# Performance work log

Measured on AMD Instinct MI355X. Metric: run time of the kernel, lower is better.

The kernel has to match this reference:

```python
import jax, jax.numpy as jnp
import numpy as np

N_P, N_W, F_IN = 512, 3584, 256
H1, O1 = 8, 32
H2, O2 = 8, 256
BATCH = 1024
NEG_SLOPE = 0.2


def _xavier(key, shape):
    fan_in, fan_out = shape[-2], shape[-1]
    lim = jnp.sqrt(6.0 / (fan_in + fan_out))
    return jax.random.uniform(key, shape, jnp.float32, -lim, lim)


def setup_inputs() -> dict:
    key = jax.random.key(0)
    ks = jax.random.split(key, 16)
    return {
        "input": jax.random.uniform(ks[0], (BATCH, N_W), jnp.float32),
        "pern_feature": jax.random.normal(ks[1], (N_P, F_IN), jnp.float32),
        "word_feature": jax.random.normal(ks[2], (N_W, F_IN), jnp.float32),
        "w1": _xavier(ks[3], (H1, F_IN, O1)),
        "a_src1": _xavier(ks[4], (H1, O1, 1)),
        "a_dst1": _xavier(ks[5], (H1, O1, 1)),
        "b1": jnp.zeros((O1,), jnp.float32),
        "w2": _xavier(ks[6], (H2, F_IN, O2)),
        "a_src2": _xavier(ks[7], (H2, F_IN, 1)),
        "a_dst2": _xavier(ks[8], (H2, F_IN, 1)),
        "b2": jnp.zeros((O2,), jnp.float32),
        "W_fc": _xavier(ks[9], (O2, 5)),
        "b_fc": jnp.zeros((5,), jnp.float32),
        "pern_adj": jax.random.randint(ks[10], (N_P, N_P), 0, 2, jnp.int32),
        "word_pern_adj": jax.random.randint(ks[11], (N_P + N_W, N_P + N_W), 0, 2, jnp.int32),
    }


def gat(h, adj, w, a_src, a_dst, bias):
    # h: [N, f_in], adj: [N, N] int, w: [H, f_in, f_out]
    h_prime = jnp.einsum('nf,hfo->hno', h, w)          # [H, N, O]
    t = jnp.tanh(h_prime)
    s_src = jnp.einsum('hno,hoi->hn', t, a_src)        # [H, N]
    s_dst = jnp.einsum('hno,hoi->hn', t, a_dst)        # [H, N]
    attn = s_src[:, :, None] + s_dst[:, None, :]       # [H, N, N]
    attn = jnp.where(attn >= 0, attn, NEG_SLOPE * attn)  # leaky_relu
    attn = jnp.where(adj[None, :, :] > 0, attn, -jnp.inf)
    attn = jax.nn.softmax(attn, axis=-1)
    out = jnp.einsum('hnm,hmo->hno', attn, h_prime)    # [H, N, O]
    return out + bias


def reference(input, pern_feature, word_feature, w1, a_src1, a_dst1, b1,
              w2, a_src2, a_dst2, b2, W_fc, b_fc, pern_adj, word_pern_adj):
    n_p = pern_feature.shape[0]
    # GAT 1 over personality graph
    h1 = gat(pern_feature, pern_adj, w1, a_src1, a_dst1, b1)       # [H1, n_p, O1]
    hiddn_pp = jnp.transpose(h1, (1, 0, 2)).reshape(n_p, -1)        # [n_p, H1*O1]
    hiddn_pp = jax.nn.elu(hiddn_pp)
    # dropout is identity in eval mode
    hiddn_wp = jnp.concatenate([word_feature, hiddn_pp], axis=0)    # [N, 256]
    h2 = gat(hiddn_wp, word_pern_adj, w2, a_src2, a_dst2, b2)       # [H2, N, O2]
    hiddn_wp2 = h2.mean(axis=0)                                     # [N, O2]
    hiddn_w = hiddn_wp2[:word_feature.shape[0], :]                  # [n_w, O2]
    x = (input @ hiddn_w) / input.sum(axis=1, keepdims=True)        # [B, O2]
    return x @ W_fc + b_fc                                          # [B, 5]
```

## Files before the change

### kernel.cpp

```cpp
#include <hip/hip_runtime.h>
#include <hip/hip_bf16.h>
#include <math.h>

#define NP 512
#define NW 3584
#define NT 4096
#define FIN 256
#define H1 8
#define O1 32
#define H2 8
#define O2 256
#define NEG 0.2f

typedef __attribute__((ext_vector_type(8))) short bf16x8;
typedef __attribute__((ext_vector_type(4))) float f32x4;
typedef __attribute__((ext_vector_type(2))) float v2f;
typedef unsigned long long u64;

__device__ __forceinline__ unsigned short f2bf(float f) {
    unsigned u = __float_as_uint(f);
    unsigned r = (u + 0x7FFF + ((u >> 16) & 1)) >> 16;
    return (unsigned short)r;
}

__device__ __forceinline__ float fast_tanh(float x) {
    float ex = __expf(2.0f * x);
    return 1.0f - 2.0f / (ex + 1.0f);
}

__global__ __launch_bounds__(256) void k_prep(
    const float* __restrict__ wf, const float* __restrict__ pf,
    const float* __restrict__ w1, const float* __restrict__ a_src1,
    const float* __restrict__ a_dst1, const float* __restrict__ w2,
    const float* __restrict__ b2, const float* __restrict__ W_fc,
    const int* __restrict__ wp_adj,
    unsigned short* __restrict__ abf, unsigned short* __restrict__ btbf,
    float* __restrict__ hp1, float* __restrict__ ss1, float* __restrict__ sd1,
    u64* __restrict__ maskT64, float* __restrict__ cvec)
{
    __shared__ float tile[64][65];
    __shared__ float feat[2][FIN];
    __shared__ float red[4][5];
    int blk = blockIdx.x;
    int t = threadIdx.x;
    if (blk < 896) {
        int idx4 = blk * 256 + t;
        float4 x = ((const float4*)wf)[idx4];
        ushort4 y;
        y.x = f2bf(x.x); y.y = f2bf(x.y); y.z = f2bf(x.z); y.w = f2bf(x.w);
        ((ushort4*)abf)[idx4] = y;
    } else if (blk < 1152) {
        int n0 = (blk - 896) * 2;
        feat[0][t] = pf[n0 * FIN + t];
        feat[1][t] = pf[(n0 + 1) * FIN + t];
        __syncthreads();
        int h = t >> 5, o = t & 31;
        float acc0 = 0.f, acc1 = 0.f;
        const float* wcol = w1 + h * FIN * O1 + o;
        #pragma unroll 4
        for (int f = 0; f < FIN; f++) {
            float w = wcol[f * O1];
            acc0 += feat[0][f] * w;
            acc1 += feat[1][f] * w;
        }
        hp1[n0 * 256 + t] = acc0;
        hp1[(n0 + 1) * 256 + t] = acc1;
        float as = a_src1[h * O1 + o];
        float ad = a_dst1[h * O1 + o];
        float accs[2] = {acc0, acc1};
        #pragma unroll
        for (int i = 0; i < 2; i++) {
            float th = tanhf(accs[i]);
            float vs = th * as, vd = th * ad;
            #pragma unroll
            for (int off = 1; off < 32; off <<= 1) {
                vs += __shfl_xor(vs, off);
                vd += __shfl_xor(vd, off);
            }
            if (o == 0) { ss1[h * NP + n0 + i] = vs; sd1[h * NP + n0 + i] = vd; }
        }
    } else if (blk < 1280) {
        int blk2 = blk - 1152;
        int h = blk2 >> 4;
        int f0 = ((blk2 >> 2) & 3) * 64;
        int o0 = (blk2 & 3) * 64;
        #pragma unroll
        for (int rr = 0; rr < 16; rr++) {
            int f = rr * 4 + (t >> 6);
            int o = t & 63;
            tile[f][o] = w2[((size_t)(h * FIN + f0 + f)) * O2 + o0 + o];
        }
        __syncthreads();
        #pragma unroll
        for (int rr = 0; rr < 16; rr++) {
            int o = rr * 4 + (t >> 6);
            int f = t & 63;
            btbf[((size_t)(h * O2 + o0 + o)) * FIN + f0 + f] = f2bf(tile[f][o]);
        }
    } else if (blk < 2176) {
        int w = t >> 6, l = t & 63;
        int r = (blk - 1280) * 4 + w;
        const int4* row = (const int4*)(wp_adj + (size_t)r * NT);
        for (int c4 = 0; c4 < 16; c4++) {
            int4 x = row[c4 * 64 + l];
            u64 nib = (u64)((x.x != 0 ? 1 : 0) | (x.y != 0 ? 2 : 0) |
                            (x.z != 0 ? 4 : 0) | (x.w != 0 ? 8 : 0));
            u64 v = nib << (4 * (l & 15));
            v |= __shfl_xor(v, 1);
            v |= __shfl_xor(v, 2);
            v |= __shfl_xor(v, 4);
            v |= __shfl_xor(v, 8);
            if ((l & 15) == 0) {
                int qw = c4 * 4 + (l >> 4);
                maskT64[(size_t)qw * NW + r] = v;
            }
        }
    } else {
        float v[5];
        #pragma unroll
        for (int j = 0; j < 5; j++) v[j] = b2[t] * W_fc[t * 5 + j];
        #pragma unroll
        for (int off = 1; off < 64; off <<= 1)
            #pragma unroll
            for (int j = 0; j < 5; j++) v[j] += __shfl_xor(v[j], off);
        int w = t >> 6, l = t & 63;
        if (l == 0) { for (int j = 0; j < 5; j++) red[w][j] = v[j]; }
        __syncthreads();
        if (t == 0)
            for (int j = 0; j < 5; j++) cvec[j] = red[0][j] + red[1][j] + red[2][j] + red[3][j];
    }
}

__global__ __launch_bounds__(256) void k_gat1_attn(
    const int* __restrict__ adj, const float* __restrict__ hp1,
    const float* __restrict__ ss1, const float* __restrict__ sd1,
    const float* __restrict__ b1, unsigned short* __restrict__ abf)
{
    __shared__ float p[2][H1][NP];
    __shared__ float den[2][H1];
    int t = threadIdx.x;
    int n0 = blockIdx.x * 2;
    for (int rr = 0; rr < 32; rr++) {
        int idx = rr * 256 + t;
        int i = idx >> 12, h = (idx >> 9) & 7, m = idx & 511;
        float a = adj[(n0 + i) * NP + m] > 0 ? 1.0f : 0.0f;
        float e = ss1[h * NP + n0 + i] + sd1[h * NP + m];
        e = fmaxf(e, NEG * e);
        p[i][h][m] = a * __expf(e);
    }
    __syncthreads();
    int w = t >> 6, l = t & 63;
    {
        int i = w & 1;
        #pragma unroll
        for (int hh = 0; hh < 4; hh++) {
            int h = (w >> 1) * 4 + hh;
            float s = 0;
            #pragma unroll
            for (int q = 0; q < 8; q++) s += p[i][h][l + 64 * q];
            #pragma unroll
            for (int off = 1; off < 64; off <<= 1) s += __shfl_xor(s, off);
            if (l == 0) den[i][h] = s;
        }
    }
    __syncthreads();
    int h = t >> 5, o = t & 31;
    float a0a = 0.f, a0b = 0.f, a1a = 0.f, a1b = 0.f;
    #pragma unroll 8
    for (int m = 0; m < NP; m += 2) {
        float v0 = hp1[m * 256 + t];
        float v1 = hp1[(m + 1) * 256 + t];
        a0a += p[0][h][m] * v0;
        a1a += p[1][h][m] * v0;
        a0b += p[0][h][m + 1] * v1;
        a1b += p[1][h][m + 1] * v1;
    }
    float acc[2] = {a0a + a0b, a1a + a1b};
    float bo = b1[o];
    #pragma unroll
    for (int i = 0; i < 2; i++) {
        float r = acc[i] / den[i][h] + bo;
        r = r > 0.f ? r : expm1f(r);
        abf[(NW + n0 + i) * FIN + t] = f2bf(r);
    }
}

__global__ __launch_bounds__(256) void k_gemm_hp2(
    const unsigned short* __restrict__ abf, const unsigned short* __restrict__ btbf,
    const float* __restrict__ a_src2, const float* __restrict__ a_dst2,
    const float* __restrict__ W_fc, float* __restrict__ gpart)
{
    __shared__ unsigned short As[128][264];
    int b = blockIdx.x;
    int nt = b & 1, h = (b >> 1) & 7, mt = b >> 4;
    int t = threadIdx.x;
    int w = t >> 6, l = t & 63;
    int m0 = mt * 128;
    {
        int row = t >> 5;
        int col8 = (t & 31) * 8;
        #pragma unroll
        for (int u = 0; u < 16; u++)
            *(bf16x8*)(&As[u * 8 + row][col8]) =
                *(const bf16x8*)(abf + (size_t)(m0 + u * 8 + row) * FIN + col8);
    }
    __syncthreads();
    int am0 = (w >> 1) * 64;
    int n0 = nt * 128 + (w & 1) * 64;
    int lr = l & 15, lq = l >> 4;
    const unsigned short* bbase = btbf + h * O2 * FIN;
    f32x4 acc[4][4];
    #pragma unroll
    for (int i = 0; i < 4; i++)
        #pragma unroll
        for (int j = 0; j < 4; j++) acc[i][j] = (f32x4){0.f, 0.f, 0.f, 0.f};
    #pragma unroll
    for (int k = 0; k < FIN; k += 32) {
        bf16x8 a[4], bf[4];
        int kc = k + lq * 8;
        #pragma unroll
        for (int j = 0; j < 4; j++)
            bf[j] = *(const bf16x8*)(bbase + (size_t)(n0 + j * 16 + lr) * FIN + kc);
        #pragma unroll
        for (int i = 0; i < 4; i++)
            a[i] = *(const bf16x8*)(&As[am0 + i * 16 + lr][kc]);
        #pragma unroll
        for (int i = 0; i < 4; i++)
            #pragma unroll
            for (int j = 0; j < 4; j++)
                acc[i][j] = __builtin_amdgcn_mfma_f32_16x16x32_bf16(a[i], bf[j], acc[i][j], 0, 0, 0);
    }
    int slice = nt * 2 + (w & 1);
    float as[4], ad[4], wfc[4][5];
    #pragma unroll
    for (int j = 0; j < 4; j++) {
        int col = n0 + j * 16 + lr;
        as[j] = a_src2[h * O2 + col];
        ad[j] = a_dst2[h * O2 + col];
        #pragma unroll
        for (int jj = 0; jj < 5; jj++) wfc[j][jj] = W_fc[col * 5 + jj];
    }
    float* base = gpart + ((size_t)h * 4 + slice) * NT * 8;
    #pragma unroll
    for (int i = 0; i < 4; i++) {
        #pragma unroll
        for (int r = 0; r < 4; r++) {
            float s[7] = {0,0,0,0,0,0,0};
            #pragma unroll
            for (int j = 0; j < 4; j++) {
                float x = acc[i][j][r];
                float th = fast_tanh(x);
                s[0] += th * as[j];
                s[1] += th * ad[j];
                #pragma unroll
                for (int jj = 0; jj < 5; jj++) s[2 + jj] += x * wfc[j][jj];
            }
            #pragma unroll
            for (int off = 1; off < 16; off <<= 1)
                #pragma unroll
                for (int q = 0; q < 7; q++) s[q] += __shfl_xor(s[q], off);
            if (lr == 0) {
                int m = m0 + am0 + i * 16 + lq * 4 + r;
                float* dst = base + (size_t)m * 8;
                #pragma unroll
                for (int q = 0; q < 7; q++) dst[q] = s[q];
            }
        }
    }
}

__global__ __launch_bounds__(256) void k_comb_hp2(
    const float* __restrict__ gpart,
    float* __restrict__ Etab, float* __restrict__ Eptab, float* __restrict__ T)
{
    int idx = blockIdx.x * 256 + threadIdx.x;
    float s[7] = {0,0,0,0,0,0,0};
    #pragma unroll
    for (int sl = 0; sl < 4; sl++) {
        const float* p = gpart + (((size_t)(idx >> 12) * 4 + sl) * NT + (idx & (NT - 1))) * 8;
        #pragma unroll
        for (int q = 0; q < 7; q++) s[q] += p[q];
    }
    Etab[idx]  = __expf(s[0]);
    Eptab[idx] = __expf(NEG * s[0]);
    float4 t0 = {__expf(s[1]), __expf(NEG * s[1]), 1.0f, s[2]};
    float4 t1 = {s[3], s[4], s[5], s[6]};
    *(float4*)(T + (size_t)idx * 8)     = t0;
    *(float4*)(T + (size_t)idx * 8 + 4) = t1;
}

__global__ __launch_bounds__(256) void k_gat2_attn(
    const u64* __restrict__ maskT64, const float* __restrict__ Etab,
    const float* __restrict__ Eptab, const float* __restrict__ T,
    float* __restrict__ part)
{
    int t = threadIdx.x;
    int w = t >> 6, l = t & 63;
    int b = blockIdx.x;
    int nb = b % 112;
    int h  = (b / 112) & 7;
    int c  = b / 896;
    int n0 = __builtin_amdgcn_readfirstlane(nb * 32 + w * 8);
    u64 epk[8];
    #pragma unroll
    for (int i = 0; i < 8; i++) {
        int r = h * NT + n0 + i;
        unsigned e  = __builtin_amdgcn_readfirstlane(__float_as_uint(Etab[r]));
        unsigned ep = __builtin_amdgcn_readfirstlane(__float_as_uint(Eptab[r]));
        epk[i] = ((u64)ep << 32) | e;
    }
    float den[8] = {0,0,0,0,0,0,0,0};
    float num[8][5] = {{0}};
    const float* Th = T + ((size_t)h * NT + c * 2048) * 8;
    for (int q = 0; q < 32; q++) {
        const float* tp = Th + (size_t)(q * 64 + l) * 8;
        f32x4 t0 = *(const f32x4*)tp;
        f32x4 t1 = *(const f32x4*)(tp + 4);
        v2f ffp = {t0.x, t0.y};
        size_t moff = (size_t)(c * 32 + q) * NW + n0;
        const u64* mq = maskT64 + moff;
        #pragma unroll
        for (int i = 0; i < 8; i++) {
            u64 wv = mq[i];
            unsigned wlo = __builtin_amdgcn_readfirstlane((unsigned)wv);
            unsigned whi = __builtin_amdgcn_readfirstlane((unsigned)(wv >> 32));
            u64 word = ((u64)whi << 32) | wlo;
            v2f pab;
            asm("v_pk_mul_f32 %0, %1, %2" : "=v"(pab) : "v"(ffp), "s"(epk[i]));
            float pp0 = fmaxf(pab.x, pab.y);
            float pp;
            asm("v_cndmask_b32 %0, 0, %1, %2" : "=v"(pp) : "v"(pp0), "s"(word));
            den[i] += pp;
            num[i][0] = fmaf(pp, t0.w, num[i][0]);
            num[i][1] = fmaf(pp, t1.x, num[i][1]);
            num[i][2] = fmaf(pp, t1.y, num[i][2]);
            num[i][3] = fmaf(pp, t1.z, num[i][3]);
            num[i][4] = fmaf(pp, t1.w, num[i][4]);
        }
    }
    #pragma unroll
    for (int i = 0; i < 8; i++) {
        float v[6];
        v[0] = den[i];
        #pragma unroll
        for (int j = 0; j < 5; j++) v[1 + j] = num[i][j];
        #pragma unroll
        for (int off = 1; off < 8; off <<= 1)
            #pragma unroll
            for (int k = 0; k < 6; k++) v[k] += __shfl_xor(v[k], off);
        if ((l & 7) == 0) {
            float* dst = part + ((((size_t)c * NW + n0 + i) * 8 + h) * 8 + (l >> 3)) * 8;
            #pragma unroll
            for (int k = 0; k < 6; k++) dst[k] = v[k];
        }
    }
}

__global__ __launch_bounds__(256) void k_gat2_comb(const float* __restrict__ part,
                                                   float* __restrict__ hf) {
    int idx = blockIdx.x * 256 + threadIdx.x;
    int n = idx >> 3, h = idx & 7;
    float den = 0, num[5] = {0,0,0,0,0};
    #pragma unroll
    for (int cc = 0; cc < 2; cc++) {
        #pragma unroll
        for (int s = 0; s < 8; s++) {
            const float* p = part + ((((size_t)cc * NW + n) * 8 + h) * 8 + s) * 8;
            float4 a = *(const float4*)p;
            float4 bq = *(const float4*)(p + 4);
            den += a.x;
            num[0] += a.y; num[1] += a.z; num[2] += a.w;
            num[3] += bq.x; num[4] += bq.y;
        }
    }
    float inv = 1.0f / (den * 8.0f);
    float v[5];
    #pragma unroll
    for (int j = 0; j < 5; j++) v[j] = num[j] * inv;
    #pragma unroll
    for (int off = 1; off < 8; off <<= 1)
        #pragma unroll
        for (int j = 0; j < 5; j++) v[j] += __shfl_xor(v[j], off);
    if (h == 0) {
        #pragma unroll
        for (int j = 0; j < 5; j++) hf[n * 5 + j] = v[j];
    }
}

__global__ __launch_bounds__(256) void k_final(
    const float* __restrict__ input, const float* __restrict__ hf,
    const float* __restrict__ cvec, const float* __restrict__ b_fc,
    float* __restrict__ out)
{
    int b = blockIdx.x, t = threadIdx.x;
    const float4* row4 = (const float4*)(input + (size_t)b * NW);
    const float4* hf4 = (const float4*)hf;
    float s = 0.f, a[5] = {0.f, 0.f, 0.f, 0.f, 0.f};
    for (int idx = t; idx < NW / 4; idx += 256) {
        float4 x = row4[idx];
        float f[20];
        #pragma unroll
        for (int q = 0; q < 5; q++) *(float4*)(f + 4 * q) = hf4[idx * 5 + q];
        s += x.x + x.y + x.z + x.w;
        #pragma unroll
        for (int j = 0; j < 5; j++)
            a[j] += x.x * f[j] + x.y * f[5 + j] + x.z * f[10 + j] + x.w * f[15 + j];
    }
    #pragma unroll
    for (int off = 1; off < 64; off <<= 1) {
        s += __shfl_xor(s, off);
        #pragma unroll
        for (int j = 0; j < 5; j++) a[j] += __shfl_xor(a[j], off);
    }
    __shared__ float red[4][6];
    int w = t >> 6, l = t & 63;
    if (l == 0) { red[w][0] = s; for (int j = 0; j < 5; j++) red[w][j + 1] = a[j]; }
    __syncthreads();
    if (t < 5) {
        float st = red[0][0] + red[1][0] + red[2][0] + red[3][0];
        float aj = red[0][t + 1] + red[1][t + 1] + red[2][t + 1] + red[3][t + 1];
        out[b * 5 + t] = aj / st + cvec[t] + b_fc[t];
    }
}

extern "C" void kernel_launch(void* const* d_in, const int* in_sizes, int n_in,
                              void* d_out, int out_size, void* d_ws, size_t ws_size,
                              hipStream_t stream) {
    const float* input   = (const float*)d_in[0];
    const float* pf      = (const float*)d_in[1];
    const float* wf      = (const float*)d_in[2];
    const float* w1      = (const float*)d_in[3];
    const float* a_src1  = (const float*)d_in[4];
    const float* a_dst1  = (const float*)d_in[5];
    const float* b1      = (const float*)d_in[6];
    const float* w2      = (const float*)d_in[7];
    const float* a_src2  = (const float*)d_in[8];
    const float* a_dst2  = (const float*)d_in[9];
    const float* b2      = (const float*)d_in[10];
    const float* W_fc    = (const float*)d_in[11];
    const float* b_fc    = (const float*)d_in[12];
    const int* pern_adj  = (const int*)d_in[13];
    const int* wp_adj    = (const int*)d_in[14];
    float* out = (float*)d_out;

    char* ws = (char*)d_ws;
    unsigned short* abf    = (unsigned short*)(ws);
    unsigned short* btbf   = (unsigned short*)(ws + 2097152);
    float*          hp1    = (float*)(ws + 3145728);
    float*          ss1    = (float*)(ws + 3670016);
    float*          sd1    = (float*)(ws + 3686400);
    float*          Etab   = (float*)(ws + 3833856);
    float*          Eptab  = (float*)(ws + 3964928);
    float*          T      = (float*)(ws + 4096000);
    float*          hf     = (float*)(ws + 5144576);
    float*          cvec   = (float*)(ws + 5216256);
    u64*            maskT64= (u64*)(ws + 5216512);
    float*          gpart  = (float*)(ws + 7051520);
    float*          part   = (float*)(ws + 11245824);

    k_prep<<<2177, 256, 0, stream>>>(wf, pf, w1, a_src1, a_dst1, w2, b2, W_fc,
                                     wp_adj, abf, btbf, hp1, ss1, sd1, maskT64, cvec);
    k_gat1_attn<<<256, 256, 0, stream>>>(pern_adj, hp1, ss1, sd1, b1, abf);
    k_gemm_hp2<<<512, 256, 0, stream>>>(abf, btbf, a_src2, a_dst2, W_fc, gpart);
    k_comb_hp2<<<128, 256, 0, stream>>>(gpart, Etab, Eptab, T);
    k_gat2_attn<<<1792, 256, 0, stream>>>(maskT64, Etab, Eptab, T, part);
    k_gat2_comb<<<112, 256, 0, stream>>>(part, hf);
    k_final<<<1024, 256, 0, stream>>>(input, hf, cvec, b_fc, out);
}
```

Measured before the change: 248.1 us.

## Transpose GAT2 mask so lanes own rows, with scalar mask loads and packed FMA

```diff
diff --git a/kernel.cpp b/kernel.cpp
--- a/kernel.cpp
+++ b/kernel.cpp
@@ -15,6 +15,7 @@
 typedef __attribute__((ext_vector_type(8))) short bf16x8;
 typedef __attribute__((ext_vector_type(4))) float f32x4;
 typedef __attribute__((ext_vector_type(2))) float v2f;
+typedef __attribute__((ext_vector_type(16))) unsigned int u32x16;
 typedef unsigned long long u64;
 
 __device__ __forceinline__ unsigned short f2bf(float f) {
@@ -36,7 +37,7 @@
     const int* __restrict__ wp_adj,
     unsigned short* __restrict__ abf, unsigned short* __restrict__ btbf,
     float* __restrict__ hp1, float* __restrict__ ss1, float* __restrict__ sd1,
-    u64* __restrict__ maskT64, float* __restrict__ cvec)
+    u64* __restrict__ maskN64, float* __restrict__ cvec)
 {
     __shared__ float tile[64][65];
     __shared__ float feat[2][FIN];
@@ -99,22 +100,18 @@
         }
     } else if (blk < 2176) {
         int w = t >> 6, l = t & 63;
-        int r = (blk - 1280) * 4 + w;
-        const int4* row = (const int4*)(wp_adj + (size_t)r * NT);
-        for (int c4 = 0; c4 < 16; c4++) {
-            int4 x = row[c4 * 64 + l];
-            u64 nib = (u64)((x.x != 0 ? 1 : 0) | (x.y != 0 ? 2 : 0) |
-                            (x.z != 0 ? 4 : 0) | (x.w != 0 ? 8 : 0));
-            u64 v = nib << (4 * (l & 15));
-            v |= __shfl_xor(v, 1);
-            v |= __shfl_xor(v, 2);
-            v |= __shfl_xor(v, 4);
-            v |= __shfl_xor(v, 8);
-            if ((l & 15) == 0) {
-                int qw = c4 * 4 + (l >> 4);
-                maskT64[(size_t)qw * NW + r] = v;
-            }
-        }
+        int tid = (blk - 1280) * 4 + w;
+        int ngrp = tid >> 6;
+        int mgrp = tid & 63;
+        const int* base = wp_adj + (size_t)(ngrp * 64) * NT + mgrp * 64 + l;
+        unsigned lo = 0, hi = 0;
+        #pragma unroll 8
+        for (int j = 0; j < 32; j++)
+            lo |= (base[(size_t)j * NT] != 0 ? 1u : 0u) << j;
+        #pragma unroll 8
+        for (int j = 0; j < 32; j++)
+            hi |= (base[(size_t)(j + 32) * NT] != 0 ? 1u : 0u) << j;
+        maskN64[(size_t)ngrp * NT + mgrp * 64 + l] = ((u64)hi << 32) | lo;
     } else {
         float v[5];
         #pragma unroll
@@ -290,93 +287,86 @@
 }
 
 __global__ __launch_bounds__(256) void k_gat2_attn(
-    const u64* __restrict__ maskT64, const float* __restrict__ Etab,
+    const u64* __restrict__ maskN64, const float* __restrict__ Etab,
     const float* __restrict__ Eptab, const float* __restrict__ T,
     float* __restrict__ part)
 {
     int t = threadIdx.x;
     int w = t >> 6, l = t & 63;
     int b = blockIdx.x;
-    int nb = b % 112;
-    int h  = (b / 112) & 7;
-    int c  = b / 896;
-    int n0 = __builtin_amdgcn_readfirstlane(nb * 32 + w * 8);
-    u64 epk[8];
-    #pragma unroll
-    for (int i = 0; i < 8; i++) {
-        int r = h * NT + n0 + i;
-        unsigned e  = __builtin_amdgcn_readfirstlane(__float_as_uint(Etab[r]));
-        unsigned ep = __builtin_amdgcn_readfirstlane(__float_as_uint(Eptab[r]));
-        epk[i] = ((u64)ep << 32) | e;
-    }
-    float den[8] = {0,0,0,0,0,0,0,0};
-    float num[8][5] = {{0}};
-    const float* Th = T + ((size_t)h * NT + c * 2048) * 8;
-    for (int q = 0; q < 32; q++) {
-        const float* tp = Th + (size_t)(q * 64 + l) * 8;
-        f32x4 t0 = *(const f32x4*)tp;
-        f32x4 t1 = *(const f32x4*)(tp + 4);
-        v2f ffp = {t0.x, t0.y};
-        size_t moff = (size_t)(c * 32 + q) * NW + n0;
-        const u64* mq = maskT64 + moff;
-        #pragma unroll
-        for (int i = 0; i < 8; i++) {
-            u64 wv = mq[i];
-            unsigned wlo = __builtin_amdgcn_readfirstlane((unsigned)wv);
-            unsigned whi = __builtin_amdgcn_readfirstlane((unsigned)(wv >> 32));
-            u64 word = ((u64)whi << 32) | wlo;
-            v2f pab;
-            asm("v_pk_mul_f32 %0, %1, %2" : "=v"(pab) : "v"(ffp), "s"(epk[i]));
-            float pp0 = fmaxf(pab.x, pab.y);
-            float pp;
-            asm("v_cndmask_b32 %0, 0, %1, %2" : "=v"(pp) : "v"(pp0), "s"(word));
-            den[i] += pp;
-            num[i][0] = fmaf(pp, t0.w, num[i][0]);
-            num[i][1] = fmaf(pp, t1.x, num[i][1]);
-            num[i][2] = fmaf(pp, t1.y, num[i][2]);
-            num[i][3] = fmaf(pp, t1.z, num[i][3]);
-            num[i][4] = fmaf(pp, t1.w, num[i][4]);
-        }
-    }
-    #pragma unroll
-    for (int i = 0; i < 8; i++) {
-        float v[6];
-        v[0] = den[i];
-        #pragma unroll
-        for (int j = 0; j < 5; j++) v[1 + j] = num[i][j];
-        #pragma unroll
-        for (int off = 1; off < 8; off <<= 1)
-            #pragma unroll
-            for (int k = 0; k < 6; k++) v[k] += __shfl_xor(v[k], off);
-        if ((l & 7) == 0) {
-            float* dst = part + ((((size_t)c * NW + n0 + i) * 8 + h) * 8 + (l >> 3)) * 8;
-            #pragma unroll
-            for (int k = 0; k < 6; k++) dst[k] = v[k];
-        }
-    }
+    int c8 = b & 7;
+    int h  = (b >> 3) & 7;
+    int ngrp = __builtin_amdgcn_readfirstlane((b >> 6) * 4 + w);
+    int n = ngrp * 64 + l;
+    v2f eE = (v2f){ Etab[h * NT + n], Eptab[h * NT + n] };
+    v2f accA = (v2f){0.f, 0.f};
+    v2f accB = (v2f){0.f, 0.f};
+    v2f accC = (v2f){0.f, 0.f};
+    const float* Tb = T + ((size_t)h * NT + c8 * 512) * 8;
+    const u64* mrow = maskN64 + (size_t)ngrp * NT + c8 * 512;
+    u32x16 mbufA, mbufB;
+    asm volatile("s_load_dwordx16 %0, %1, 0x0" : "=s"(mbufA) : "s"(mrow));
+    #define G2BODY(G, BUF)                                                            \
+    {                                                                                 \
+        const float* tg = Tb + (size_t)(G) * 64;                                      \
+        _Pragma("unroll")                                                             \
+        for (int k = 0; k < 8; k++) {                                                 \
+            v2f ffp = *(const v2f*)(tg + k * 8);                        \
+            v2f g10 = *(const v2f*)(tg + k * 8 + 2);                    \
+            v2f g21 = *(const v2f*)(tg + k * 8 + 4);                    \
+            v2f g43 = *(const v2f*)(tg + k * 8 + 6);                    \
+            u64 word = ((u64)BUF[2 * k + 1] << 32) | (u64)BUF[2 * k];                 \
+            v2f pab;                                                                  \
+            asm("v_pk_mul_f32 %0, %1, %2" : "=v"(pab) : "v"(ffp), "v"(eE));           \
+            float pp0 = fmaxf(pab.x, pab.y);                   \
+            float ppl, pph;                                                           \
+            asm("v_cndmask_b32 %0, 0, %1, %2" : "=v"(ppl) : "v"(pp0), "s"(word));     \
+            asm("v_cndmask_b32 %0, 0, %1, %2" : "=v"(pph) : "v"(pp0), "s"(word));     \
+            v2f ppv = (v2f){ppl, pph};                                                \
+            asm("v_pk_fma_f32 %0, %1, %2, %0" : "+v"(accA) : "v"(ppv), "v"(g10));     \
+            asm("v_pk_fma_f32 %0, %1, %2, %0" : "+v"(accB) : "v"(ppv), "v"(g21));     \
+            asm("v_pk_fma_f32 %0, %1, %2, %0" : "+v"(accC) : "v"(ppv), "v"(g43));     \
+        }                                                                             \
+    }
+    for (int g = 0; g < 64; g += 2) {
+        asm volatile("s_waitcnt lgkmcnt(0)");
+        __builtin_amdgcn_sched_barrier(0);
+        {
+            const u64* mp = mrow + (size_t)(g + 1) * 8;
+            asm volatile("s_load_dwordx16 %0, %1, 0x0" : "=s"(mbufB) : "s"(mp));
+        }
+        G2BODY(g, mbufA)
+        asm volatile("s_waitcnt lgkmcnt(0)");
+        __builtin_amdgcn_sched_barrier(0);
+        {
+            const u64* mp = mrow + (size_t)((g + 2) & 63) * 8;
+            asm volatile("s_load_dwordx16 %0, %1, 0x0" : "=s"(mbufA) : "s"(mp));
+        }
+        G2BODY(g + 1, mbufB)
+    }
+    #undef G2BODY
+    part[((size_t)(0 * 8 + c8) * 8 + h) * NW + n] = accA.x;
+    part[((size_t)(1 * 8 + c8) * 8 + h) * NW + n] = accA.y;
+    part[((size_t)(2 * 8 + c8) * 8 + h) * NW + n] = accB.x;
+    part[((size_t)(3 * 8 + c8) * 8 + h) * NW + n] = accB.y;
+    part[((size_t)(4 * 8 + c8) * 8 + h) * NW + n] = accC.x;
+    part[((size_t)(5 * 8 + c8) * 8 + h) * NW + n] = accC.y;
 }
 
 __global__ __launch_bounds__(256) void k_gat2_comb(const float* __restrict__ part,
                                                    float* __restrict__ hf) {
     int idx = blockIdx.x * 256 + threadIdx.x;
     int n = idx >> 3, h = idx & 7;
-    float den = 0, num[5] = {0,0,0,0,0};
-    #pragma unroll
-    for (int cc = 0; cc < 2; cc++) {
-        #pragma unroll
-        for (int s = 0; s < 8; s++) {
-            const float* p = part + ((((size_t)cc * NW + n) * 8 + h) * 8 + s) * 8;
-            float4 a = *(const float4*)p;
-            float4 bq = *(const float4*)(p + 4);
-            den += a.x;
-            num[0] += a.y; num[1] += a.z; num[2] += a.w;
-            num[3] += bq.x; num[4] += bq.y;
-        }
-    }
-    float inv = 1.0f / (den * 8.0f);
+    float s[6] = {0, 0, 0, 0, 0, 0};
+    #pragma unroll
+    for (int c = 0; c < 8; c++)
+        #pragma unroll
+        for (int k = 0; k < 6; k++)
+            s[k] += part[((size_t)(k * 8 + c) * 8 + h) * NW + n];
+    float inv = 1.0f / (s[0] * 8.0f);
     float v[5];
     #pragma unroll
-    for (int j = 0; j < 5; j++) v[j] = num[j] * inv;
+    for (int j = 0; j < 5; j++) v[j] = s[1 + j] * inv;
     #pragma unroll
     for (int off = 1; off < 8; off <<= 1)
         #pragma unroll
@@ -454,16 +444,16 @@
     float*          T      = (float*)(ws + 4096000);
     float*          hf     = (float*)(ws + 5144576);
     float*          cvec   = (float*)(ws + 5216256);
-    u64*            maskT64= (u64*)(ws + 5216512);
+    u64*            maskN64= (u64*)(ws + 5216512);
     float*          gpart  = (float*)(ws + 7051520);
     float*          part   = (float*)(ws + 11245824);
 
     k_prep<<<2177, 256, 0, stream>>>(wf, pf, w1, a_src1, a_dst1, w2, b2, W_fc,
-                                     wp_adj, abf, btbf, hp1, ss1, sd1, maskT64, cvec);
+                                     wp_adj, abf, btbf, hp1, ss1, sd1, maskN64, cvec);
     k_gat1_attn<<<256, 256, 0, stream>>>(pern_adj, hp1, ss1, sd1, b1, abf);
     k_gemm_hp2<<<512, 256, 0, stream>>>(abf, btbf, a_src2, a_dst2, W_fc, gpart);
     k_comb_hp2<<<128, 256, 0, stream>>>(gpart, Etab, Eptab, T);
-    k_gat2_attn<<<1792, 256, 0, stream>>>(maskT64, Etab, Eptab, T, part);
+    k_gat2_attn<<<896, 256, 0, stream>>>(maskN64, Etab, Eptab, T, part);
     k_gat2_comb<<<112, 256, 0, stream>>>(part, hf);
     k_final<<<1024, 256, 0, stream>>>(input, hf, cvec, b_fc, out);
 }
```

Measured after the change: 280.5 us. 13.1% more time.
